# Kernel optimization log

Measured on AMD Instinct MI355X. Metric: run time of the kernel, lower is better.

Reference implementation:

```python
import jax, jax.numpy as jnp
import numpy as np

OUT, IN = 11008, 4096
GROUP = 128
NUM_GROUPS = IN // GROUP  # 32
PACKED = OUT * IN // 2
TOKENS = 4096


def setup_inputs() -> dict:
    key = jax.random.key(0)
    k1, k2, k3, k4 = jax.random.split(key, 4)
    x = jax.random.normal(k1, (TOKENS, IN), dtype=jnp.float32)
    # packed bytes: two int4 values per byte (low nibble = even index)
    w_packed = jax.random.randint(k2, (PACKED,), 0, 256, dtype=jnp.int32)
    # per-(out_channel, group) scale and integer zero-point
    w_scale = jax.random.uniform(k3, (OUT, NUM_GROUPS), dtype=jnp.float32) * 0.02 + 1e-3
    w_zero = jax.random.randint(k4, (OUT, NUM_GROUPS), 0, 16, dtype=jnp.int32)
    return {"x": x, "w_packed": w_packed, "w_scale": w_scale, "w_zero": w_zero}


def _dequant_weight(w_packed, w_scale, w_zero):
    out_features, num_groups = w_scale.shape
    in_features = (w_packed.shape[0] * 2) // out_features
    group = in_features // num_groups
    # unpack nibbles: element 2i -> low nibble, element 2i+1 -> high nibble
    low = w_packed & 15
    high = (w_packed >> 4) & 15
    w4 = jnp.stack([low, high], axis=-1).reshape(out_features, in_features)
    # signed int4: values >= 8 map to value - 16
    w4 = jnp.where(w4 >= 8, w4 - 16, w4).astype(jnp.float32)
    # per-group dequant: (w - zero) * scale
    wg = w4.reshape(out_features, num_groups, group)
    w = (wg - w_zero.astype(jnp.float32)[:, :, None]) * w_scale[:, :, None]
    return w.reshape(out_features, in_features)


def reference(x, w_packed, w_scale, w_zero):
    w = _dequant_weight(w_packed, w_scale, w_zero)  # [OUT, IN]
    return x @ w.T  # [TOKENS, OUT]
```

## Files before the change

kernel.cpp:

```cpp
#include <hip/hip_runtime.h>
#include <stdint.h>
#include <stddef.h>


#define M_TOK 4096
#define K_IN  4096
#define N_OUT 11008
#define NGRP  32

#define MTI 16
#define NTI 43
#define TILES (MTI * NTI)

#define BH_OFF ((size_t)M_TOK * K_IN * 2)

typedef _Float16 h8v __attribute__((ext_vector_type(8)));
typedef float    f4v __attribute__((ext_vector_type(4)));

__device__ __forceinline__ void gload16(const void* g, void* l) {
  __builtin_amdgcn_global_load_lds(
      (__attribute__((address_space(1))) void*)(g),
      (__attribute__((address_space(3))) void*)(l),
      16, 0, 0);
}

#define MEMFENCE asm volatile("" ::: "memory")
__device__ __forceinline__ void bar() {
  MEMFENCE;
  __builtin_amdgcn_s_barrier();
  MEMFENCE;
}
#define WAIT_VM4 asm volatile("s_waitcnt vmcnt(4)" ::: "memory")

__global__ __launch_bounds__(256) void cvt_x_kernel(const float* __restrict__ x,
                                                    _Float16* __restrict__ xh) {
  size_t t = (size_t)blockIdx.x * 256 + threadIdx.x;
  const float4* s = (const float4*)x + t * 2;
  float4 a = s[0], b = s[1];
  h8v o;
  o[0] = (_Float16)a.x; o[1] = (_Float16)a.y; o[2] = (_Float16)a.z; o[3] = (_Float16)a.w;
  o[4] = (_Float16)b.x; o[5] = (_Float16)b.y; o[6] = (_Float16)b.z; o[7] = (_Float16)b.w;
  ((h8v*)xh)[t] = o;
}

__global__ __launch_bounds__(256) void dequant_w_kernel(const int* __restrict__ wp,
                                                        const float* __restrict__ ws,
                                                        const int* __restrict__ wz,
                                                        _Float16* __restrict__ bh) {
  size_t tg = (size_t)blockIdx.x * 256 + threadIdx.x;
  int j   = (int)(tg & 127);
  int row = (int)(tg >> 7);
  int g = j >> 2;
  float s = ws[(size_t)row * NGRP + g];
  float c = -s * (8.0f + (float)wz[(size_t)row * NGRP + g]);
  const int4* src = (const int4*)(wp + (size_t)row * 2048 + j * 16);
  _Float16* dst = bh + (size_t)row * 4096 + j * 32;
#pragma unroll
  for (int b = 0; b < 4; ++b) {
    int4 v = src[b];
    int q[4] = {v.x, v.y, v.z, v.w};
    h8v o;
#pragma unroll
    for (int i = 0; i < 4; ++i) {
      int lo = (q[i] & 15) ^ 8;
      int hi = ((q[i] >> 4) & 15) ^ 8;
      o[2 * i]     = (_Float16)(s * (float)lo + c);
      o[2 * i + 1] = (_Float16)(s * (float)hi + c);
    }
    ((h8v*)dst)[b] = o;
  }
}

__global__ __launch_bounds__(512, 2) void gemm_kernel(
    const _Float16* __restrict__ Ah,
    const _Float16* __restrict__ Bh,
    float* __restrict__ C) {
  __shared__ __align__(128) char smem[131072];

  const int bid = blockIdx.x;
  const int swz = (bid & 7) * 86 + (bid >> 3);
  const int mt = swz / NTI;
  const int nt = swz - mt * NTI;
  const int m0 = mt * 256;
  const int n0 = nt * 256;

  const int tid  = threadIdx.x;
  const int lane = tid & 63;
  const int wid  = tid >> 6;
  const int wm   = wid >> 2;
  const int wn   = wid & 3;
  const int lrow = lane & 15;
  const int quad = lane >> 4;

  const int r0 = wid * 32 + (lane >> 2);
  const int kc = (lane & 3) ^ ((lane >> 3) & 3);
  const size_t gA0 = (size_t)(m0 + r0) * K_IN + kc * 8;
  const size_t gB0 = (size_t)(n0 + r0) * K_IN + kc * 8;
  const int ldsl = wid * 2048;

  const int su   = quad ^ ((lrow >> 1) & 3);
  const int aoff = ((wm * 128 + lrow) * 4 + su) * 16;
  const int boff = 32768 + ((wn * 64 + lrow) * 4 + su) * 16;

  f4v acc[8][4];
#pragma unroll
  for (int i = 0; i < 8; ++i)
#pragma unroll
    for (int j = 0; j < 4; ++j) acc[i][j] = (f4v){0.f, 0.f, 0.f, 0.f};

  h8v af_a[4], af_b[4], bf_a[4], bf_b[4];

#define STAGE4(NXT, KT, KH)                                                    \
  { const _Float16* gA_ = Ah + gA0 + (size_t)(KT) * 64 + (KH) * 32;            \
    const _Float16* gB_ = Bh + gB0 + (size_t)(KT) * 64 + (KH) * 32;            \
    char* lA_ = smem + (NXT) * 65536 + (KH) * 16384 + ldsl;                    \
    gload16(gA_, lA_);                                                         \
    gload16(gA_ + 16 * K_IN, lA_ + 1024);                                      \
    gload16(gB_, lA_ + 32768);                                                 \
    gload16(gB_ + 16 * K_IN, lA_ + 32768 + 1024); }

#define RD_AF(DST, BUF, SEC, MH)                                               \
  { const char* s_ = smem + (BUF) * 65536 + (SEC) * 16384;                     \
    _Pragma("unroll")                                                          \
    for (int i_ = 0; i_ < 4; ++i_)                                             \
      DST[i_] = *(const h8v*)(s_ + aoff + (MH) * 4096 + i_ * 1024); }

#define RD_BF(DST, BUF, SEC)                                                   \
  { const char* s_ = smem + (BUF) * 65536 + (SEC) * 16384;                     \
    _Pragma("unroll")                                                          \
    for (int i_ = 0; i_ < 4; ++i_)                                             \
      DST[i_] = *(const h8v*)(s_ + boff + i_ * 1024); }

#define MFMA16(AF, BF, MH)                                                     \
  { __builtin_amdgcn_s_setprio(1);                                             \
    _Pragma("unroll")                                                          \
    for (int mi_ = 0; mi_ < 4; ++mi_)                                          \
      _Pragma("unroll")                                                        \
      for (int nf_ = 0; nf_ < 4; ++nf_)                                        \
        acc[(MH) * 4 + mi_][nf_] = __builtin_amdgcn_mfma_f32_16x16x32_f16(     \
            AF[mi_], BF[nf_], acc[(MH) * 4 + mi_][nf_], 0, 0, 0);              \
    __builtin_amdgcn_s_setprio(0); }

  STAGE4(0, 0, 0);
  STAGE4(0, 0, 1);
  WAIT_VM4;
  bar();
  RD_AF(af_a, 0, 0, 0);
  RD_BF(bf_a, 0, 0);

  for (int t = 0; t < 64; t += 2) {
    const int t1 = t + 1;
    const int t2 = (t + 2 < 64) ? t + 2 : 63;
    RD_AF(af_b, 0, 0, 1); STAGE4(1, t1, 0); MFMA16(af_a, bf_a, 0); WAIT_VM4; bar();
    RD_AF(af_a, 0, 1, 0); RD_BF(bf_b, 0, 1); MFMA16(af_b, bf_a, 1); bar();
    RD_AF(af_b, 0, 1, 1); STAGE4(1, t1, 1); MFMA16(af_a, bf_b, 0); WAIT_VM4; bar();
    RD_AF(af_a, 1, 0, 0); RD_BF(bf_a, 1, 0); MFMA16(af_b, bf_b, 1); bar();
    RD_AF(af_b, 1, 0, 1); STAGE4(0, t2, 0); MFMA16(af_a, bf_a, 0); WAIT_VM4; bar();
    RD_AF(af_a, 1, 1, 0); RD_BF(bf_b, 1, 1); MFMA16(af_b, bf_a, 1); bar();
    RD_AF(af_b, 1, 1, 1); STAGE4(0, t2, 1); MFMA16(af_a, bf_b, 0); WAIT_VM4; bar();
    RD_AF(af_a, 0, 0, 0); RD_BF(bf_a, 0, 0); MFMA16(af_b, bf_b, 1); bar();
  }

#pragma unroll
  for (int mf = 0; mf < 8; ++mf) {
#pragma unroll
    for (int rr = 0; rr < 4; ++rr) {
      int m = m0 + wm * 128 + mf * 16 + quad * 4 + rr;
      float* crow = C + (size_t)m * N_OUT + n0 + wn * 64 + lrow;
#pragma unroll
      for (int nf = 0; nf < 4; ++nf) crow[nf * 16] = acc[mf][nf][rr];
    }
  }
#undef MFMA16
#undef RD_BF
#undef RD_AF
#undef STAGE4
}

extern "C" void kernel_launch(void* const* d_in, const int* in_sizes, int n_in,
                              void* d_out, int out_size, void* d_ws, size_t ws_size,
                              hipStream_t stream) {
  const float* x   = (const float*)d_in[0];
  const int*   wp  = (const int*)d_in[1];
  const float* wsc = (const float*)d_in[2];
  const int*   wz  = (const int*)d_in[3];

  _Float16* Ah = (_Float16*)d_ws;
  _Float16* Bh = (_Float16*)((char*)d_ws + BH_OFF);

  cvt_x_kernel<<<(M_TOK * (size_t)K_IN) / (8 * 256), 256, 0, stream>>>(x, Ah);
  dequant_w_kernel<<<((size_t)N_OUT * 128) / 256, 256, 0, stream>>>(wp, wsc, wz, Bh);
  gemm_kernel<<<TILES, 512, 0, stream>>>(Ah, Bh, (float*)d_out);
}
```

Before: 647.0 us.

## Restructure GEMM main loop into per-phase LDS-read, barrier, MFMA schedule

```diff
diff --git a/kernel.cpp b/kernel.cpp
--- a/kernel.cpp
+++ b/kernel.cpp
@@ -24,13 +24,11 @@
       16, 0, 0);
 }
 
-#define MEMFENCE asm volatile("" ::: "memory")
-__device__ __forceinline__ void bar() {
-  MEMFENCE;
-  __builtin_amdgcn_s_barrier();
-  MEMFENCE;
-}
-#define WAIT_VM4 asm volatile("s_waitcnt vmcnt(4)" ::: "memory")
+#define WAIT_VM4 asm volatile("s_waitcnt vmcnt(4)")
+#define LGKM0_SB0                                                              \
+  { asm volatile("s_waitcnt lgkmcnt(0)");                                      \
+    __builtin_amdgcn_sched_barrier(0); }
+#define BAR __builtin_amdgcn_s_barrier()
 
 __global__ __launch_bounds__(256) void cvt_x_kernel(const float* __restrict__ x,
                                                     _Float16* __restrict__ xh) {
@@ -108,7 +106,7 @@
 #pragma unroll
     for (int j = 0; j < 4; ++j) acc[i][j] = (f4v){0.f, 0.f, 0.f, 0.f};
 
-  h8v af_a[4], af_b[4], bf_a[4], bf_b[4];
+  h8v af[4], bf[4];
 
 #define STAGE4(NXT, KT, KH)                                                    \
   { const _Float16* gA_ = Ah + gA0 + (size_t)(KT) * 64 + (KH) * 32;            \
@@ -119,46 +117,48 @@
     gload16(gB_, lA_ + 32768);                                                 \
     gload16(gB_ + 16 * K_IN, lA_ + 32768 + 1024); }
 
-#define RD_AF(DST, BUF, SEC, MH)                                               \
-  { const char* s_ = smem + (BUF) * 65536 + (SEC) * 16384;                     \
+#define PHASE(CUR, SEC, MH, DO_STAGE, DO_VM)                                   \
+  {                                                                            \
+    const char* sec_ = smem + (CUR) * 65536 + (SEC) * 16384;                   \
+    if ((MH) == 0) {                                                           \
+      _Pragma("unroll")                                                        \
+      for (int nf_ = 0; nf_ < 4; ++nf_)                                        \
+        bf[nf_] = *(const h8v*)(sec_ + boff + nf_ * 1024);                     \
+    }                                                                          \
     _Pragma("unroll")                                                          \
     for (int i_ = 0; i_ < 4; ++i_)                                             \
-      DST[i_] = *(const h8v*)(s_ + aoff + (MH) * 4096 + i_ * 1024); }
-
-#define RD_BF(DST, BUF, SEC)                                                   \
-  { const char* s_ = smem + (BUF) * 65536 + (SEC) * 16384;                     \
-    _Pragma("unroll")                                                          \
-    for (int i_ = 0; i_ < 4; ++i_)                                             \
-      DST[i_] = *(const h8v*)(s_ + boff + i_ * 1024); }
-
-#define MFMA16(AF, BF, MH)                                                     \
-  { __builtin_amdgcn_s_setprio(1);                                             \
+      af[i_] = *(const h8v*)(sec_ + aoff + (MH) * 4096 + i_ * 1024);           \
+    DO_STAGE;                                                                  \
+    BAR;                                                                       \
+    LGKM0_SB0;                                                                 \
+    __builtin_amdgcn_s_setprio(1);                                             \
     _Pragma("unroll")                                                          \
     for (int mi_ = 0; mi_ < 4; ++mi_)                                          \
       _Pragma("unroll")                                                        \
       for (int nf_ = 0; nf_ < 4; ++nf_)                                        \
         acc[(MH) * 4 + mi_][nf_] = __builtin_amdgcn_mfma_f32_16x16x32_f16(     \
-            AF[mi_], BF[nf_], acc[(MH) * 4 + mi_][nf_], 0, 0, 0);              \
-    __builtin_amdgcn_s_setprio(0); }
+            af[mi_], bf[nf_], acc[(MH) * 4 + mi_][nf_], 0, 0, 0);              \
+    __builtin_amdgcn_s_setprio(0);                                             \
+    if (DO_VM) { WAIT_VM4; }                                                   \
+    BAR;                                                                       \
+  }
 
   STAGE4(0, 0, 0);
   STAGE4(0, 0, 1);
   WAIT_VM4;
-  bar();
-  RD_AF(af_a, 0, 0, 0);
-  RD_BF(bf_a, 0, 0);
+  BAR;
 
   for (int t = 0; t < 64; t += 2) {
     const int t1 = t + 1;
     const int t2 = (t + 2 < 64) ? t + 2 : 63;
-    RD_AF(af_b, 0, 0, 1); STAGE4(1, t1, 0); MFMA16(af_a, bf_a, 0); WAIT_VM4; bar();
-    RD_AF(af_a, 0, 1, 0); RD_BF(bf_b, 0, 1); MFMA16(af_b, bf_a, 1); bar();
-    RD_AF(af_b, 0, 1, 1); STAGE4(1, t1, 1); MFMA16(af_a, bf_b, 0); WAIT_VM4; bar();
-    RD_AF(af_a, 1, 0, 0); RD_BF(bf_a, 1, 0); MFMA16(af_b, bf_b, 1); bar();
-    RD_AF(af_b, 1, 0, 1); STAGE4(0, t2, 0); MFMA16(af_a, bf_a, 0); WAIT_VM4; bar();
-    RD_AF(af_a, 1, 1, 0); RD_BF(bf_b, 1, 1); MFMA16(af_b, bf_a, 1); bar();
-    RD_AF(af_b, 1, 1, 1); STAGE4(0, t2, 1); MFMA16(af_a, bf_b, 0); WAIT_VM4; bar();
-    RD_AF(af_a, 0, 0, 0); RD_BF(bf_a, 0, 0); MFMA16(af_b, bf_b, 1); bar();
+    PHASE(0, 0, 0, STAGE4(1, t1, 0), 0)
+    PHASE(0, 0, 1, {},                1)
+    PHASE(0, 1, 0, STAGE4(1, t1, 1), 0)
+    PHASE(0, 1, 1, {},                1)
+    PHASE(1, 0, 0, STAGE4(0, t2, 0), 0)
+    PHASE(1, 0, 1, {},                1)
+    PHASE(1, 1, 0, STAGE4(0, t2, 1), 0)
+    PHASE(1, 1, 1, {},                1)
   }
 
 #pragma unroll
@@ -171,9 +171,7 @@
       for (int nf = 0; nf < 4; ++nf) crow[nf * 16] = acc[mf][nf][rr];
     }
   }
-#undef MFMA16
-#undef RD_BF
-#undef RD_AF
+#undef PHASE
 #undef STAGE4
 }
 
```

New measurement: 645.6 us. No clear change (-0.2%).
